# Performance work log

Measured on AMD Instinct MI355X. Metric: run time of the kernel, lower is better.

The kernel has to match this reference:

```python
import jax, jax.numpy as jnp
import numpy as np
import math

NUM_HEADS = 16
D_MODEL = 1024
B, T = 1, 4096


def setup_inputs() -> dict:
    key = jax.random.key(0)
    kx, kq, kk, kv, ko = jax.random.split(key, 5)
    s = 1.0 / math.sqrt(D_MODEL)
    return {
        "x": jax.random.normal(kx, (B, T, D_MODEL), dtype=jnp.float32),
        "Wq": jax.random.normal(kq, (D_MODEL, D_MODEL), dtype=jnp.float32) * s,
        "Wk": jax.random.normal(kk, (D_MODEL, D_MODEL), dtype=jnp.float32) * s,
        "Wv": jax.random.normal(kv, (D_MODEL, D_MODEL), dtype=jnp.float32) * s,
        "Wo": jax.random.normal(ko, (D_MODEL, D_MODEL), dtype=jnp.float32) * s,
    }


def reference(x, Wq, Wk, Wv, Wo):
    # x: (B, T, D); weights stored torch-Linear style: y = x @ W.T
    Bx, Tx, D = x.shape
    H = NUM_HEADS
    dk = D // H
    q = (x @ Wq.T).reshape(Bx, Tx, H, dk)  # (B,T,H,dk)
    k = (x @ Wk.T).reshape(Bx, Tx, H, dk)
    v = (x @ Wv.T).reshape(Bx, Tx, H, dk)
    # scores: (B,H,T,T), scaled dot-product
    scores = jnp.einsum("bthd,bshd->bhts", q, k) / math.sqrt(dk)
    causal_mask = jnp.triu(jnp.ones((Tx, Tx), dtype=bool), k=1)  # True above diag
    scores = jnp.where(causal_mask, jnp.float32(-jnp.inf), scores).astype(jnp.float32)
    attn = jax.nn.softmax(scores, axis=-1)  # fp32 softmax, as in the torch module
    out = jnp.einsum("bhts,bshd->bthd", attn, v).reshape(Bx, Tx, D)
    return out @ Wo.T
```

## Files before the change

kernel.cpp:

```cpp
#include <hip/hip_runtime.h>
#include <hip/hip_bf16.h>
#include <math.h>

typedef __attribute__((ext_vector_type(8)))  __bf16 bf16x8;
typedef __attribute__((ext_vector_type(4)))  __bf16 bf16x4;
typedef __attribute__((ext_vector_type(4)))  float  f32x4;
typedef __attribute__((ext_vector_type(16))) float  f32x16;

static constexpr int T_SEQ = 4096;
static constexpr int DM    = 1024;
static constexpr int NH    = 16;
static constexpr int C2_QB    = 22;
static constexpr int C3_QB    = 44;
static constexpr int SPL_ROWS = T_SEQ - C2_QB * 64;
static constexpr int C3_ROWS  = T_SEQ - C3_QB * 64;
static constexpr int NY = 126;
static constexpr float QSCALE = 0.125f * 1.44269504088896340736f;

__device__ __forceinline__ void gload16(const void* g, void* l) {
    __builtin_amdgcn_global_load_lds(
        (const __attribute__((address_space(1))) unsigned int*)g,
        (__attribute__((address_space(3))) unsigned int*)l,
        16, 0, 0);
}

__device__ __forceinline__ unsigned cvtpk_bf16(float a, float b) {
    unsigned r;
    asm("v_cvt_pk_bf16_f32 %0, %1, %2" : "=v"(r) : "v"(a), "v"(b));
    return r;
}
__device__ __forceinline__ void permswap(unsigned& x, unsigned& y) {
    asm("v_permlane32_swap_b32 %0, %1" : "+v"(x), "+v"(y));
}
__device__ __forceinline__ float xhalf_max(float v) {
    union { float f; unsigned u; } a, b;
    a.f = v; b.f = v;
    asm volatile("" : "+v"(b.u));
    permswap(a.u, b.u);
    return fmaxf(a.f, b.f);
}
__device__ __forceinline__ float xhalf_sum(float v) {
    union { float f; unsigned u; } a, b;
    a.f = v; b.f = v;
    asm volatile("" : "+v"(b.u));
    permswap(a.u, b.u);
    return a.f + b.f;
}

__global__ __launch_bounds__(256)
void cvt_bf16(const float* __restrict__ in, __bf16* __restrict__ out, int n4) {
    int i = blockIdx.x * blockDim.x + threadIdx.x;
    if (i >= n4) return;
    float4 v = ((const float4*)in)[i];
    bf16x4 o;
    o[0] = (__bf16)v.x; o[1] = (__bf16)v.y; o[2] = (__bf16)v.z; o[3] = (__bf16)v.w;
    ((bf16x4*)out)[i] = o;
}

__global__ __launch_bounds__(256)
void cvt4_bf16(const float* __restrict__ a0, const float* __restrict__ a1,
               const float* __restrict__ a2, const float* __restrict__ a3,
               __bf16* __restrict__ o0, __bf16* __restrict__ o1,
               __bf16* __restrict__ o2, __bf16* __restrict__ o3, int n4) {
    int i = blockIdx.x * blockDim.x + threadIdx.x;
    if (i >= n4) return;
    const float* in = blockIdx.y == 0 ? a0 : blockIdx.y == 1 ? a1 : blockIdx.y == 2 ? a2 : a3;
    __bf16* out     = blockIdx.y == 0 ? o0 : blockIdx.y == 1 ? o1 : blockIdx.y == 2 ? o2 : o3;
    float4 v = ((const float4*)in)[i];
    bf16x4 o;
    o[0] = (__bf16)v.x; o[1] = (__bf16)v.y; o[2] = (__bf16)v.z; o[3] = (__bf16)v.w;
    ((bf16x4*)out)[i] = o;
}

template<bool OUT_BF16>
__device__ __forceinline__ void gemm_body(const __bf16* __restrict__ A,
                                          const __bf16* __restrict__ B,
                                          void* __restrict__ Cout,
                                          int N, int K, float scale,
                                          int bx, int by) {
    __shared__ __align__(16) __bf16 Al[128 * 64];
    __shared__ __align__(16) __bf16 Bl[128 * 64];
    const int tid  = threadIdx.x;
    const int lane = tid & 63;
    const int wid  = tid >> 6;
    const int wr   = wid >> 1, wc = wid & 1;
    const int m0   = by * 128, n0 = bx * 128;
    const int r    = lane & 15, g = lane >> 4;

    f32x4 acc[4][4];
    const f32x4 z4 = {0.f, 0.f, 0.f, 0.f};
    #pragma unroll
    for (int i = 0; i < 4; ++i)
        #pragma unroll
        for (int j = 0; j < 4; ++j) acc[i][j] = z4;

    for (int kt = 0; kt < K; kt += 64) {
        __syncthreads();
        #pragma unroll
        for (int p = 0; p < 4; ++p) {
            int u    = p * 256 + tid;
            int row  = u >> 3;
            int col8 = (u & 7) ^ (row & 7);
            gload16(A + (size_t)(m0 + row) * K + kt + col8 * 8,
                    (char*)Al + (p * 256 + wid * 64) * 16);
            gload16(B + (size_t)(n0 + row) * K + kt + col8 * 8,
                    (char*)Bl + (p * 256 + wid * 64) * 16);
        }
        __syncthreads();
        __builtin_amdgcn_s_setprio(1);
        #pragma unroll
        for (int kk = 0; kk < 2; ++kk) {
            bf16x8 af[4], bfr[4];
            #pragma unroll
            for (int mi = 0; mi < 4; ++mi)
                af[mi] = *(const bf16x8*)&Al[(wr * 64 + mi * 16 + r) * 64 + (((kk * 4 + g) ^ (r & 7)) * 8)];
            #pragma unroll
            for (int nj = 0; nj < 4; ++nj)
                bfr[nj] = *(const bf16x8*)&Bl[(wc * 64 + nj * 16 + r) * 64 + (((kk * 4 + g) ^ (r & 7)) * 8)];
            #pragma unroll
            for (int mi = 0; mi < 4; ++mi)
                #pragma unroll
                for (int nj = 0; nj < 4; ++nj)
                    acc[mi][nj] = __builtin_amdgcn_mfma_f32_16x16x32_bf16(af[mi], bfr[nj], acc[mi][nj], 0, 0, 0);
        }
        __builtin_amdgcn_s_setprio(0);
    }
    #pragma unroll
    for (int mi = 0; mi < 4; ++mi)
        #pragma unroll
        for (int nj = 0; nj < 4; ++nj)
            #pragma unroll
            for (int j = 0; j < 4; ++j) {
                int row = m0 + wr * 64 + mi * 16 + g * 4 + j;
                int col = n0 + wc * 64 + nj * 16 + r;
                float v = acc[mi][nj][j] * scale;
                if (OUT_BF16) ((__bf16*)Cout)[(size_t)row * N + col] = (__bf16)v;
                else          ((float*)Cout)[(size_t)row * N + col]  = v;
            }
}

__global__ __launch_bounds__(256)
void gemm_qkv(const __bf16* __restrict__ A,
              const __bf16* __restrict__ W0, const __bf16* __restrict__ W1,
              const __bf16* __restrict__ W2,
              __bf16* __restrict__ O0, __bf16* __restrict__ O1, __bf16* __restrict__ O2) {
    const int z = blockIdx.z;
    const __bf16* B = z == 0 ? W0 : (z == 1 ? W1 : W2);
    __bf16*       C = z == 0 ? O0 : (z == 1 ? O1 : O2);
    float scale = z == 0 ? QSCALE : 1.0f;
    gemm_body<true>(A, B, C, DM, DM, scale, blockIdx.x, blockIdx.y);
}

__global__ __launch_bounds__(256)
void gemm_out(const __bf16* __restrict__ A, const __bf16* __restrict__ B,
              float* __restrict__ C) {
    gemm_body<false>(A, B, C, DM, DM, 1.0f, blockIdx.x, blockIdx.y);
}

__global__ __launch_bounds__(256)
void vtrans(const __bf16* __restrict__ V, __bf16* __restrict__ Vt) {
    __shared__ __bf16 tl[64][72];
    const int tid = threadIdx.x;
    const int t0  = blockIdx.x * 64;
    const int h   = blockIdx.y;
    #pragma unroll
    for (int p = 0; p < 2; ++p) {
        int c = p * 256 + tid, row = c >> 3, col8 = c & 7;
        *(bf16x8*)&tl[row][col8 * 8] =
            *(const bf16x8*)(V + (size_t)(t0 + row) * DM + h * 64 + col8 * 8);
    }
    __syncthreads();
    #pragma unroll
    for (int p = 0; p < 2; ++p) {
        int c = p * 256 + tid, d = c >> 3, tc8 = c & 7;
        bf16x8 o;
        #pragma unroll
        for (int e = 0; e < 8; ++e) o[e] = tl[tc8 * 8 + e][d];
        *(bf16x8*)(Vt + (size_t)(h * 64 + d) * T_SEQ + t0 + tc8 * 8) = o;
    }
}

__global__ __launch_bounds__(128)
void attn_fwd(const __bf16* __restrict__ Q, const __bf16* __restrict__ Kp,
              const __bf16* __restrict__ Vt, __bf16* __restrict__ O,
              __bf16* __restrict__ U0, __bf16* __restrict__ U1,
              __bf16* __restrict__ U2, float* __restrict__ Ml)
{
    __shared__ __align__(16) __bf16 Kl[2][64 * 64];
    __shared__ __align__(16) __bf16 Vl[2][64 * 64];
    const int tid  = threadIdx.x;
    const int lane = tid & 63, wid = tid >> 6;
    const int l31  = lane & 31;
    const int hi   = lane >> 5;
    const int h    = blockIdx.x;
    const int y    = blockIdx.y;
    int qb, chunk, nc;
    if (y < 60)       { qb = 63 - y / 3;        chunk = y % 3;        nc = 3; }
    else if (y < 104) { int s = y - 60; qb = 43 - s / 2; chunk = s % 2; nc = 2; }
    else              { qb = 21 - (y - 104);    chunk = 0;            nc = 1; }
    const int n    = qb + 1;
    const int base = n / nc, rem = n % nc;
    const int t0i  = chunk * base + (chunk < rem ? chunk : rem);
    const int t1i  = t0i + base + (chunk < rem ? 1 : 0) - 1;
    const int qw = qb * 64 + wid * 32;
    const int qg = qw + l31;

    bf16x8 qf[4];
    #pragma unroll
    for (int kd0 = 0; kd0 < 4; ++kd0)
        qf[kd0] = *(const bf16x8*)(Q + (size_t)qg * DM + h * 64 + kd0 * 16 + hi * 8);

    float m_i = -1e30f, l_i = 0.f;
    f32x16 oacc[2];
    #pragma unroll
    for (int d = 0; d < 2; ++d)
        #pragma unroll
        for (int e = 0; e < 16; ++e) oacc[d][e] = 0.f;

    auto stage_lds = [&](int t, int buf) {
        #pragma unroll
        for (int p = 0; p < 4; ++p) {
            int u    = p * 128 + tid;
            int row  = u >> 3;
            int col8 = (u & 7) ^ (row & 7);
            gload16(Kp + (size_t)(t * 64 + row) * DM + h * 64 + col8 * 8,
                    (char*)&Kl[buf][0] + (p * 128 + wid * 64) * 16);
            gload16(Vt + (size_t)(h * 64 + row) * T_SEQ + t * 64 + col8 * 8,
                    (char*)&Vl[buf][0] + (p * 128 + wid * 64) * 16);
        }
    };
    stage_lds(t0i, 0);
    if (t1i > t0i) stage_lds(t0i + 1, 1);
    __syncthreads();

    auto qk = [&](f32x16* sdst, int buf) {
        #pragma unroll
        for (int ksub = 0; ksub < 2; ++ksub) {
            const int row = ksub * 32 + l31;
            f32x16 a;
            #pragma unroll
            for (int e = 0; e < 16; ++e) a[e] = 0.f;
            #pragma unroll
            for (int kd0 = 0; kd0 < 4; ++kd0) {
                bf16x8 kf = *(const bf16x8*)
                    &Kl[buf][(row << 6) + ((((kd0 << 1) + hi) ^ (row & 7)) << 3)];
                a = __builtin_amdgcn_mfma_f32_32x32x16_bf16(kf, qf[kd0], a, 0, 0, 0);
            }
            sdst[ksub] = a;
        }
    };
    auto mask_sf = [&](f32x16* s, int t) {
        const int kb = (t << 6) + 4 * hi;
        #pragma unroll
        for (int ksub = 0; ksub < 2; ++ksub)
            #pragma unroll
            for (int e = 0; e < 16; ++e) {
                int k = kb + ksub * 32 + ((e & 3) + 8 * (e >> 2));
                if (k > qg) s[ksub][e] = -1e30f;
            }
    };

    f32x16 sf[2], sfn[2];
    qk(sf, 0);
    if (t0i == qb) mask_sf(sf, t0i);

    bf16x8 kreg[4], vreg[4];
    for (int t = t0i; t <= t1i; ++t) {
        const int cur = (t - t0i) & 1;
        const bool have_next  = (t + 1 <= t1i);
        const bool have_next2 = (t + 2 <= t1i);
        if (have_next2) {
            const int t2 = t + 2;
            #pragma unroll
            for (int p = 0; p < 4; ++p) {
                int u   = p * 128 + tid;
                int row = u >> 3;
                int c   = u & 7;
                kreg[p] = *(const bf16x8*)(Kp + (size_t)(t2 * 64 + row) * DM + h * 64 + c * 8);
                vreg[p] = *(const bf16x8*)(Vt + (size_t)(h * 64 + row) * T_SEQ + t2 * 64 + c * 8);
            }
        }
        __builtin_amdgcn_s_setprio(1);
        if (have_next) {
            qk(sfn, cur ^ 1);
            if (t + 1 == qb) mask_sf(sfn, t + 1);
        }
        __builtin_amdgcn_s_setprio(0);
        float pm;
        {
            float t0[8];
            #pragma unroll
            for (int e = 0; e < 8; ++e)
                t0[e] = fmaxf(fmaxf(sf[0][e], sf[0][e + 8]), fmaxf(sf[1][e], sf[1][e + 8]));
            #pragma unroll
            for (int s = 4; s > 0; s >>= 1)
                #pragma unroll
                for (int e = 0; e < s; ++e) t0[e] = fmaxf(t0[e], t0[e + s]);
            pm = xhalf_max(t0[0]);
        }
        if (pm > m_i + 8.f) {
            float al = exp2f(m_i - pm);
            m_i = pm;
            l_i *= al;
            #pragma unroll
            for (int d = 0; d < 2; ++d)
                #pragma unroll
                for (int e = 0; e < 16; ++e) oacc[d][e] *= al;
        }
        float p[32];
        #pragma unroll
        for (int i = 0; i < 32; ++i)
            p[i] = exp2f(sf[i >> 4][i & 15] - m_i);
        {
            float s0[8];
            #pragma unroll
            for (int e = 0; e < 8; ++e)
                s0[e] = (p[e] + p[e + 8]) + (p[e + 16] + p[e + 24]);
            #pragma unroll
            for (int s = 4; s > 0; s >>= 1)
                #pragma unroll
                for (int e = 0; e < s; ++e) s0[e] += s0[e + s];
            l_i += xhalf_sum(s0[0]);
        }
        __builtin_amdgcn_s_setprio(1);
        #pragma unroll
        for (int ks = 0; ks < 4; ++ks) {
            unsigned w0 = cvtpk_bf16(p[8 * ks + 0], p[8 * ks + 1]);
            unsigned w1 = cvtpk_bf16(p[8 * ks + 2], p[8 * ks + 3]);
            unsigned w2 = cvtpk_bf16(p[8 * ks + 4], p[8 * ks + 5]);
            unsigned w3 = cvtpk_bf16(p[8 * ks + 6], p[8 * ks + 7]);
            permswap(w0, w2);
            permswap(w1, w3);
            union { unsigned u[4]; bf16x8 v; } pu;
            pu.u[0] = w0; pu.u[1] = w1; pu.u[2] = w2; pu.u[3] = w3;
            #pragma unroll
            for (int dsub = 0; dsub < 2; ++dsub) {
                const int row = dsub * 32 + l31;
                bf16x8 vt = *(const bf16x8*)
                    &Vl[cur][(row << 6) + ((((ks << 1) + hi) ^ (row & 7)) << 3)];
                oacc[dsub] = __builtin_amdgcn_mfma_f32_32x32x16_bf16(vt, pu.v, oacc[dsub], 0, 0, 0);
            }
        }
        __builtin_amdgcn_s_setprio(0);
        if (have_next2) {
            __syncthreads();
            #pragma unroll
            for (int p = 0; p < 4; ++p) {
                int u   = p * 128 + tid;
                int row = u >> 3;
                int c   = u & 7;
                *(bf16x8*)&Kl[cur][(row << 6) + ((c ^ (row & 7)) << 3)] = kreg[p];
                *(bf16x8*)&Vl[cur][(row << 6) + ((c ^ (row & 7)) << 3)] = vreg[p];
            }
            __syncthreads();
        }
        if (have_next) {
            sf[0] = sfn[0];
            sf[1] = sfn[1];
        }
    }
    __syncthreads();
    __bf16* ow = &Kl[0][0] + wid * 2048;
    const float invl = (nc > 1) ? 1.0f : (1.f / l_i);
    #pragma unroll
    for (int dsub = 0; dsub < 2; ++dsub)
        #pragma unroll
        for (int e = 0; e < 16; ++e) {
            int d = dsub * 32 + ((e & 3) + 8 * (e >> 2)) + 4 * hi;
            float v = oacc[dsub][e] * invl;
            int bo = l31 * 128 + ((2 * d) ^ ((l31 & 7) << 4));
            *(__bf16*)((char*)ow + bo) = (__bf16)v;
        }
    if (nc == 1) {
        #pragma unroll
        for (int i = 0; i < 4; ++i) {
            int u  = hi * 4 + i;
            int bo = l31 * 128 + ((u * 16) ^ ((l31 & 7) << 4));
            bf16x8 v8 = *(const bf16x8*)((char*)ow + bo);
            *(bf16x8*)(O + (size_t)qg * DM + h * 64 + u * 8) = v8;
        }
    } else {
        __bf16* Uc = (chunk == 0) ? U0 : (chunk == 1) ? U1 : U2;
        const int rows  = (chunk == 2) ? C3_ROWS : SPL_ROWS;
        const int ridx  = qg - ((chunk == 2) ? C3_QB * 64 : C2_QB * 64);
        #pragma unroll
        for (int i = 0; i < 4; ++i) {
            int u  = hi * 4 + i;
            int bo = l31 * 128 + ((u * 16) ^ ((l31 & 7) << 4));
            bf16x8 v8 = *(const bf16x8*)((char*)ow + bo);
            *(bf16x8*)(Uc + ((size_t)h * rows + ridx) * 64 + u * 8) = v8;
        }
        if (hi == 0) {
            size_t off = (chunk == 0) ? ((size_t)h * SPL_ROWS + (qg - C2_QB * 64))
                       : (chunk == 1) ? ((size_t)NH * SPL_ROWS + (size_t)h * SPL_ROWS + (qg - C2_QB * 64))
                                      : ((size_t)2 * NH * SPL_ROWS + (size_t)h * C3_ROWS + (qg - C3_QB * 64));
            float* mlp = Ml + off * 2;
            mlp[0] = m_i;
            mlp[1] = l_i;
        }
    }
}

__global__ __launch_bounds__(256)
void attn_combine(const __bf16* __restrict__ U0, const __bf16* __restrict__ U1,
                  const __bf16* __restrict__ U2, const float* __restrict__ Ml,
                  __bf16* __restrict__ O) {
    int gid = blockIdx.x * 256 + threadIdx.x;
    int rh  = gid >> 3;
    int e8  = gid & 7;
    int ridx = rh >> 4, h = rh & 15;
    int qg   = C2_QB * 64 + ridx;
    bool has3 = (qg >= C3_QB * 64);
    const float* ml0 = Ml + ((size_t)h * SPL_ROWS + ridx) * 2;
    const float* ml1 = Ml + ((size_t)NH * SPL_ROWS + (size_t)h * SPL_ROWS + ridx) * 2;
    float m0 = ml0[0], l0 = ml0[1], m1 = ml1[0], l1 = ml1[1];
    float m2 = -1e30f, l2 = 0.f;
    if (has3) {
        const float* ml2 = Ml + ((size_t)2 * NH * SPL_ROWS
                                 + (size_t)h * C3_ROWS + (qg - C3_QB * 64)) * 2;
        m2 = ml2[0]; l2 = ml2[1];
    }
    float M  = fmaxf(fmaxf(m0, m1), m2);
    float s0 = exp2f(m0 - M), s1 = exp2f(m1 - M);
    float s2 = has3 ? exp2f(m2 - M) : 0.f;
    float inv = 1.f / (l0 * s0 + l1 * s1 + l2 * s2);
    bf16x8 u0 = *(const bf16x8*)(U0 + ((size_t)h * SPL_ROWS + ridx) * 64 + e8 * 8);
    bf16x8 u1 = *(const bf16x8*)(U1 + ((size_t)h * SPL_ROWS + ridx) * 64 + e8 * 8);
    bf16x8 o;
    if (has3) {
        bf16x8 u2 = *(const bf16x8*)(U2 + ((size_t)h * C3_ROWS + (qg - C3_QB * 64)) * 64 + e8 * 8);
        #pragma unroll
        for (int j = 0; j < 8; ++j)
            o[j] = (__bf16)((((float)u0[j] * s0 + (float)u1[j] * s1) + (float)u2[j] * s2) * inv);
    } else {
        #pragma unroll
        for (int j = 0; j < 8; ++j)
            o[j] = (__bf16)(((float)u0[j] * s0 + (float)u1[j] * s1) * inv);
    }
    *(bf16x8*)(O + (size_t)qg * DM + h * 64 + e8 * 8) = o;
}

extern "C" void kernel_launch(void* const* d_in, const int* in_sizes, int n_in,
                              void* d_out, int out_size, void* d_ws, size_t ws_size,
                              hipStream_t stream) {
    const float* x  = (const float*)d_in[0];
    const float* Wq = (const float*)d_in[1];
    const float* Wk = (const float*)d_in[2];
    const float* Wv = (const float*)d_in[3];
    const float* Wo = (const float*)d_in[4];
    float* out = (float*)d_out;

    char* ws = (char*)d_ws;
    const size_t MB = (size_t)1 << 20;
    __bf16* xb    = (__bf16*)(ws + 0 * MB);
    __bf16* U0B   = (__bf16*)(ws + 0 * MB);
    __bf16* wqb   = (__bf16*)(ws + 8 * MB);
    float*  MlB   = (float*)(ws + 8 * MB);
    __bf16* wkb   = (__bf16*)(ws + 10 * MB);
    __bf16* U2B   = (__bf16*)(ws + 10 * MB);
    __bf16* wvb   = (__bf16*)(ws + 12 * MB);
    __bf16* wob   = (__bf16*)(ws + 14 * MB);
    __bf16* Qb    = (__bf16*)(ws + 16 * MB);
    __bf16* Kb    = (__bf16*)(ws + 24 * MB);
    __bf16* Vb    = (__bf16*)(ws + 32 * MB);
    __bf16* U1B   = (__bf16*)(ws + 32 * MB);
    __bf16* attnb = (__bf16*)(ws + 40 * MB);
    __bf16* VtG   = (__bf16*)(ws + 0 * MB);
    __bf16* VtR   = (__bf16*)(ws + 48 * MB);

    const int nX = T_SEQ * DM / 4;
    const int nW = DM * DM / 4;
    cvt_bf16<<<(nX + 255) / 256, 256, 0, stream>>>(x, xb, nX);
    cvt4_bf16<<<dim3((nW + 255) / 256, 4), 256, 0, stream>>>(Wq, Wk, Wv, Wo,
                                                             wqb, wkb, wvb, wob, nW);

    gemm_qkv<<<dim3(DM / 128, T_SEQ / 128, 3), 256, 0, stream>>>(xb, wqb, wkb, wvb, Qb, Kb, Vb);

    vtrans<<<dim3(T_SEQ / 64, NH), 256, 0, stream>>>(Vb, VtR);

    attn_fwd<<<dim3(NH, NY), 128, 0, stream>>>(Qb, Kb, VtR, attnb, U0B, U1B, U2B, MlB);

    attn_combine<<<(SPL_ROWS * NH * 8) / 256, 256, 0, stream>>>(U0B, U1B, U2B, MlB, attnb);

    gemm_out<<<dim3(DM / 128, T_SEQ / 128), 256, 0, stream>>>(attnb, wob, out);
}
```

Before: 163.5 us.

## Use 128-row query blocks with four waves sharing each K/V tile

The attention kernel now gives each workgroup a 128-query block, served by four waves of 256 threads, in place of a 64-query block with two waves. Each staged K/V tile in LDS is therefore reused by twice as many queries, which halves K/V global and LDS staging traffic per query and halves the grid. Waves whose queries lie entirely above a diagonal tile skip the QK and PV work for it through a per-wave guard. The split-chunk assignment is remapped for the coarser blocks. The risks are fewer workgroups and less occupancy, plus load imbalance, because near the diagonal some waves sit idle while others in the same block do work.

```diff
diff --git a/kernel.cpp b/kernel.cpp
--- a/kernel.cpp
+++ b/kernel.cpp
@@ -14,7 +14,7 @@
 static constexpr int C3_QB    = 44;
 static constexpr int SPL_ROWS = T_SEQ - C2_QB * 64;
 static constexpr int C3_ROWS  = T_SEQ - C3_QB * 64;
-static constexpr int NY = 126;
+static constexpr int NY = 63;
 static constexpr float QSCALE = 0.125f * 1.44269504088896340736f;
 
 __device__ __forceinline__ void gload16(const void* g, void* l) {
@@ -180,7 +180,7 @@
     }
 }
 
-__global__ __launch_bounds__(128)
+__global__ __launch_bounds__(256)
 void attn_fwd(const __bf16* __restrict__ Q, const __bf16* __restrict__ Kp,
               const __bf16* __restrict__ Vt, __bf16* __restrict__ O,
               __bf16* __restrict__ U0, __bf16* __restrict__ U1,
@@ -194,16 +194,16 @@
     const int hi   = lane >> 5;
     const int h    = blockIdx.x;
     const int y    = blockIdx.y;
-    int qb, chunk, nc;
-    if (y < 60)       { qb = 63 - y / 3;        chunk = y % 3;        nc = 3; }
-    else if (y < 104) { int s = y - 60; qb = 43 - s / 2; chunk = s % 2; nc = 2; }
-    else              { qb = 21 - (y - 104);    chunk = 0;            nc = 1; }
-    const int n    = qb + 1;
+    int qblk, chunk, nc;
+    if (y < 30)      { qblk = 31 - y / 3;       chunk = y % 3;        nc = 3; }
+    else if (y < 52) { int s = y - 30; qblk = 21 - s / 2; chunk = s % 2; nc = 2; }
+    else             { qblk = 10 - (y - 52);    chunk = 0;            nc = 1; }
+    const int n    = 2 * qblk + 2;
     const int base = n / nc, rem = n % nc;
     const int t0i  = chunk * base + (chunk < rem ? chunk : rem);
     const int t1i  = t0i + base + (chunk < rem ? 1 : 0) - 1;
-    const int qw = qb * 64 + wid * 32;
-    const int qg = qw + l31;
+    const int qw   = qblk * 128 + wid * 32;
+    const int qg   = qw + l31;
 
     bf16x8 qf[4];
     #pragma unroll
@@ -219,14 +219,14 @@
 
     auto stage_lds = [&](int t, int buf) {
         #pragma unroll
-        for (int p = 0; p < 4; ++p) {
-            int u    = p * 128 + tid;
+        for (int p = 0; p < 2; ++p) {
+            int u    = p * 256 + tid;
             int row  = u >> 3;
             int col8 = (u & 7) ^ (row & 7);
             gload16(Kp + (size_t)(t * 64 + row) * DM + h * 64 + col8 * 8,
-                    (char*)&Kl[buf][0] + (p * 128 + wid * 64) * 16);
+                    (char*)&Kl[buf][0] + (p * 256 + wid * 64) * 16);
             gload16(Vt + (size_t)(h * 64 + row) * T_SEQ + t * 64 + col8 * 8,
-                    (char*)&Vl[buf][0] + (p * 128 + wid * 64) * 16);
+                    (char*)&Vl[buf][0] + (p * 256 + wid * 64) * 16);
         }
     };
     stage_lds(t0i, 0);
@@ -259,12 +259,15 @@
                 if (k > qg) s[ksub][e] = -1e30f;
             }
     };
+    auto haswork = [&](int t) { return (t << 6) <= qw + 31; };
 
     f32x16 sf[2], sfn[2];
-    qk(sf, 0);
-    if (t0i == qb) mask_sf(sf, t0i);
-
-    bf16x8 kreg[4], vreg[4];
+    if (haswork(t0i)) {
+        qk(sf, 0);
+        if ((t0i << 6) + 63 > qw) mask_sf(sf, t0i);
+    }
+
+    bf16x8 kreg[2], vreg[2];
     for (int t = t0i; t <= t1i; ++t) {
         const int cur = (t - t0i) & 1;
         const bool have_next  = (t + 1 <= t1i);
@@ -272,8 +275,8 @@
         if (have_next2) {
             const int t2 = t + 2;
             #pragma unroll
-            for (int p = 0; p < 4; ++p) {
-                int u   = p * 128 + tid;
+            for (int p = 0; p < 2; ++p) {
+                int u   = p * 256 + tid;
                 int row = u >> 3;
                 int c   = u & 7;
                 kreg[p] = *(const bf16x8*)(Kp + (size_t)(t2 * 64 + row) * DM + h * 64 + c * 8);
@@ -281,72 +284,74 @@
             }
         }
         __builtin_amdgcn_s_setprio(1);
-        if (have_next) {
+        if (have_next && haswork(t + 1)) {
             qk(sfn, cur ^ 1);
-            if (t + 1 == qb) mask_sf(sfn, t + 1);
+            if (((t + 1) << 6) + 63 > qw) mask_sf(sfn, t + 1);
         }
         __builtin_amdgcn_s_setprio(0);
-        float pm;
-        {
-            float t0[8];
-            #pragma unroll
-            for (int e = 0; e < 8; ++e)
-                t0[e] = fmaxf(fmaxf(sf[0][e], sf[0][e + 8]), fmaxf(sf[1][e], sf[1][e + 8]));
-            #pragma unroll
-            for (int s = 4; s > 0; s >>= 1)
-                #pragma unroll
-                for (int e = 0; e < s; ++e) t0[e] = fmaxf(t0[e], t0[e + s]);
-            pm = xhalf_max(t0[0]);
-        }
-        if (pm > m_i + 8.f) {
-            float al = exp2f(m_i - pm);
-            m_i = pm;
-            l_i *= al;
-            #pragma unroll
-            for (int d = 0; d < 2; ++d)
-                #pragma unroll
-                for (int e = 0; e < 16; ++e) oacc[d][e] *= al;
-        }
-        float p[32];
-        #pragma unroll
-        for (int i = 0; i < 32; ++i)
-            p[i] = exp2f(sf[i >> 4][i & 15] - m_i);
-        {
-            float s0[8];
-            #pragma unroll
-            for (int e = 0; e < 8; ++e)
-                s0[e] = (p[e] + p[e + 8]) + (p[e + 16] + p[e + 24]);
-            #pragma unroll
-            for (int s = 4; s > 0; s >>= 1)
-                #pragma unroll
-                for (int e = 0; e < s; ++e) s0[e] += s0[e + s];
-            l_i += xhalf_sum(s0[0]);
-        }
-        __builtin_amdgcn_s_setprio(1);
-        #pragma unroll
-        for (int ks = 0; ks < 4; ++ks) {
-            unsigned w0 = cvtpk_bf16(p[8 * ks + 0], p[8 * ks + 1]);
-            unsigned w1 = cvtpk_bf16(p[8 * ks + 2], p[8 * ks + 3]);
-            unsigned w2 = cvtpk_bf16(p[8 * ks + 4], p[8 * ks + 5]);
-            unsigned w3 = cvtpk_bf16(p[8 * ks + 6], p[8 * ks + 7]);
-            permswap(w0, w2);
-            permswap(w1, w3);
-            union { unsigned u[4]; bf16x8 v; } pu;
-            pu.u[0] = w0; pu.u[1] = w1; pu.u[2] = w2; pu.u[3] = w3;
-            #pragma unroll
-            for (int dsub = 0; dsub < 2; ++dsub) {
-                const int row = dsub * 32 + l31;
-                bf16x8 vt = *(const bf16x8*)
-                    &Vl[cur][(row << 6) + ((((ks << 1) + hi) ^ (row & 7)) << 3)];
-                oacc[dsub] = __builtin_amdgcn_mfma_f32_32x32x16_bf16(vt, pu.v, oacc[dsub], 0, 0, 0);
-            }
-        }
-        __builtin_amdgcn_s_setprio(0);
+        if (haswork(t)) {
+            float pm;
+            {
+                float t0[8];
+                #pragma unroll
+                for (int e = 0; e < 8; ++e)
+                    t0[e] = fmaxf(fmaxf(sf[0][e], sf[0][e + 8]), fmaxf(sf[1][e], sf[1][e + 8]));
+                #pragma unroll
+                for (int s = 4; s > 0; s >>= 1)
+                    #pragma unroll
+                    for (int e = 0; e < s; ++e) t0[e] = fmaxf(t0[e], t0[e + s]);
+                pm = xhalf_max(t0[0]);
+            }
+            if (pm > m_i + 8.f) {
+                float al = exp2f(m_i - pm);
+                m_i = pm;
+                l_i *= al;
+                #pragma unroll
+                for (int d = 0; d < 2; ++d)
+                    #pragma unroll
+                    for (int e = 0; e < 16; ++e) oacc[d][e] *= al;
+            }
+            float p[32];
+            #pragma unroll
+            for (int i = 0; i < 32; ++i)
+                p[i] = exp2f(sf[i >> 4][i & 15] - m_i);
+            {
+                float s0[8];
+                #pragma unroll
+                for (int e = 0; e < 8; ++e)
+                    s0[e] = (p[e] + p[e + 8]) + (p[e + 16] + p[e + 24]);
+                #pragma unroll
+                for (int s = 4; s > 0; s >>= 1)
+                    #pragma unroll
+                    for (int e = 0; e < s; ++e) s0[e] += s0[e + s];
+                l_i += xhalf_sum(s0[0]);
+            }
+            __builtin_amdgcn_s_setprio(1);
+            #pragma unroll
+            for (int ks = 0; ks < 4; ++ks) {
+                unsigned w0 = cvtpk_bf16(p[8 * ks + 0], p[8 * ks + 1]);
+                unsigned w1 = cvtpk_bf16(p[8 * ks + 2], p[8 * ks + 3]);
+                unsigned w2 = cvtpk_bf16(p[8 * ks + 4], p[8 * ks + 5]);
+                unsigned w3 = cvtpk_bf16(p[8 * ks + 6], p[8 * ks + 7]);
+                permswap(w0, w2);
+                permswap(w1, w3);
+                union { unsigned u[4]; bf16x8 v; } pu;
+                pu.u[0] = w0; pu.u[1] = w1; pu.u[2] = w2; pu.u[3] = w3;
+                #pragma unroll
+                for (int dsub = 0; dsub < 2; ++dsub) {
+                    const int row = dsub * 32 + l31;
+                    bf16x8 vt = *(const bf16x8*)
+                        &Vl[cur][(row << 6) + ((((ks << 1) + hi) ^ (row & 7)) << 3)];
+                    oacc[dsub] = __builtin_amdgcn_mfma_f32_32x32x16_bf16(vt, pu.v, oacc[dsub], 0, 0, 0);
+                }
+            }
+            __builtin_amdgcn_s_setprio(0);
+        }
         if (have_next2) {
             __syncthreads();
             #pragma unroll
-            for (int p = 0; p < 4; ++p) {
-                int u   = p * 128 + tid;
+            for (int p = 0; p < 2; ++p) {
+                int u   = p * 256 + tid;
                 int row = u >> 3;
                 int c   = u & 7;
                 *(bf16x8*)&Kl[cur][(row << 6) + ((c ^ (row & 7)) << 3)] = kreg[p];
@@ -391,9 +396,9 @@
             *(bf16x8*)(Uc + ((size_t)h * rows + ridx) * 64 + u * 8) = v8;
         }
         if (hi == 0) {
-            size_t off = (chunk == 0) ? ((size_t)h * SPL_ROWS + (qg - C2_QB * 64))
-                       : (chunk == 1) ? ((size_t)NH * SPL_ROWS + (size_t)h * SPL_ROWS + (qg - C2_QB * 64))
-                                      : ((size_t)2 * NH * SPL_ROWS + (size_t)h * C3_ROWS + (qg - C3_QB * 64));
+            size_t off = (chunk == 0) ? ((size_t)h * SPL_ROWS + ridx)
+                       : (chunk == 1) ? ((size_t)(NH + h) * SPL_ROWS + ridx)
+                                      : ((size_t)2 * NH * SPL_ROWS + (size_t)h * C3_ROWS + ridx);
             float* mlp = Ml + off * 2;
             mlp[0] = m_i;
             mlp[1] = l_i;
@@ -412,7 +417,7 @@
     int qg   = C2_QB * 64 + ridx;
     bool has3 = (qg >= C3_QB * 64);
     const float* ml0 = Ml + ((size_t)h * SPL_ROWS + ridx) * 2;
-    const float* ml1 = Ml + ((size_t)NH * SPL_ROWS + (size_t)h * SPL_ROWS + ridx) * 2;
+    const float* ml1 = Ml + ((size_t)(NH + h) * SPL_ROWS + ridx) * 2;
     float m0 = ml0[0], l0 = ml0[1], m1 = ml1[0], l1 = ml1[1];
     float m2 = -1e30f, l2 = 0.f;
     if (has3) {
@@ -465,7 +470,6 @@
     __bf16* Vb    = (__bf16*)(ws + 32 * MB);
     __bf16* U1B   = (__bf16*)(ws + 32 * MB);
     __bf16* attnb = (__bf16*)(ws + 40 * MB);
-    __bf16* VtG   = (__bf16*)(ws + 0 * MB);
     __bf16* VtR   = (__bf16*)(ws + 48 * MB);
 
     const int nX = T_SEQ * DM / 4;
@@ -478,7 +482,7 @@
 
     vtrans<<<dim3(T_SEQ / 64, NH), 256, 0, stream>>>(Vb, VtR);
 
-    attn_fwd<<<dim3(NH, NY), 128, 0, stream>>>(Qb, Kb, VtR, attnb, U0B, U1B, U2B, MlB);
+    attn_fwd<<<dim3(NH, NY), 256, 0, stream>>>(Qb, Kb, VtR, attnb, U0B, U1B, U2B, MlB);
 
     attn_combine<<<(SPL_ROWS * NH * 8) / 256, 256, 0, stream>>>(U0B, U1B, U2B, MlB, attnb);
 
```

Result: slower. 202.8 us (+24.0%).

## Merge conversion kernels and single-buffer K tile in attention LDS

Applied to the files above, without the earlier changes.

Fuses the x and weight fp32-to-bf16 conversions into one launch with a 5-slice grid, removing a kernel launch at the cost of many idle blocks in the weight slices. In the attention kernel, K is now held in a single LDS buffer and the next K tile is loaded into registers and written only after the current QK is consumed, cutting LDS use so more blocks can fit per CU. This adds extra barriers in the prologue and ties K staging more tightly to the compute loop, which may expose load latency. Index expressions for the Ml offsets are simplified.

```diff
diff --git a/kernel.cpp b/kernel.cpp
--- a/kernel.cpp
+++ b/kernel.cpp
@@ -48,24 +48,18 @@
 }
 
 __global__ __launch_bounds__(256)
-void cvt_bf16(const float* __restrict__ in, __bf16* __restrict__ out, int n4) {
+void cvt5_bf16(const float* __restrict__ a0, const float* __restrict__ a1,
+               const float* __restrict__ a2, const float* __restrict__ a3,
+               const float* __restrict__ a4,
+               __bf16* __restrict__ o0, __bf16* __restrict__ o1,
+               __bf16* __restrict__ o2, __bf16* __restrict__ o3,
+               __bf16* __restrict__ o4, int nX4, int nW4) {
+    int y = blockIdx.y;
+    int n4 = (y == 0) ? nX4 : nW4;
     int i = blockIdx.x * blockDim.x + threadIdx.x;
     if (i >= n4) return;
-    float4 v = ((const float4*)in)[i];
-    bf16x4 o;
-    o[0] = (__bf16)v.x; o[1] = (__bf16)v.y; o[2] = (__bf16)v.z; o[3] = (__bf16)v.w;
-    ((bf16x4*)out)[i] = o;
-}
-
-__global__ __launch_bounds__(256)
-void cvt4_bf16(const float* __restrict__ a0, const float* __restrict__ a1,
-               const float* __restrict__ a2, const float* __restrict__ a3,
-               __bf16* __restrict__ o0, __bf16* __restrict__ o1,
-               __bf16* __restrict__ o2, __bf16* __restrict__ o3, int n4) {
-    int i = blockIdx.x * blockDim.x + threadIdx.x;
-    if (i >= n4) return;
-    const float* in = blockIdx.y == 0 ? a0 : blockIdx.y == 1 ? a1 : blockIdx.y == 2 ? a2 : a3;
-    __bf16* out     = blockIdx.y == 0 ? o0 : blockIdx.y == 1 ? o1 : blockIdx.y == 2 ? o2 : o3;
+    const float* in = y == 0 ? a0 : y == 1 ? a1 : y == 2 ? a2 : y == 3 ? a3 : a4;
+    __bf16* out     = y == 0 ? o0 : y == 1 ? o1 : y == 2 ? o2 : y == 3 ? o3 : o4;
     float4 v = ((const float4*)in)[i];
     bf16x4 o;
     o[0] = (__bf16)v.x; o[1] = (__bf16)v.y; o[2] = (__bf16)v.z; o[3] = (__bf16)v.w;
@@ -186,7 +180,7 @@
               __bf16* __restrict__ U0, __bf16* __restrict__ U1,
               __bf16* __restrict__ U2, float* __restrict__ Ml)
 {
-    __shared__ __align__(16) __bf16 Kl[2][64 * 64];
+    __shared__ __align__(16) __bf16 Kl[64 * 64];
     __shared__ __align__(16) __bf16 Vl[2][64 * 64];
     const int tid  = threadIdx.x;
     const int lane = tid & 63, wid = tid >> 6;
@@ -217,23 +211,43 @@
         #pragma unroll
         for (int e = 0; e < 16; ++e) oacc[d][e] = 0.f;
 
-    auto stage_lds = [&](int t, int buf) {
+    bf16x8 kreg[4], vreg[4];
+    auto stageK_lds = [&](int t) {
         #pragma unroll
         for (int p = 0; p < 4; ++p) {
             int u    = p * 128 + tid;
             int row  = u >> 3;
             int col8 = (u & 7) ^ (row & 7);
             gload16(Kp + (size_t)(t * 64 + row) * DM + h * 64 + col8 * 8,
-                    (char*)&Kl[buf][0] + (p * 128 + wid * 64) * 16);
+                    (char*)&Kl[0] + (p * 128 + wid * 64) * 16);
+        }
+    };
+    auto stageV_lds = [&](int t, int buf) {
+        #pragma unroll
+        for (int p = 0; p < 4; ++p) {
+            int u    = p * 128 + tid;
+            int row  = u >> 3;
+            int col8 = (u & 7) ^ (row & 7);
             gload16(Vt + (size_t)(h * 64 + row) * T_SEQ + t * 64 + col8 * 8,
                     (char*)&Vl[buf][0] + (p * 128 + wid * 64) * 16);
         }
     };
-    stage_lds(t0i, 0);
-    if (t1i > t0i) stage_lds(t0i + 1, 1);
-    __syncthreads();
-
-    auto qk = [&](f32x16* sdst, int buf) {
+    auto ldK = [&](int t) {
+        #pragma unroll
+        for (int p = 0; p < 4; ++p) {
+            int u = p * 128 + tid, row = u >> 3, c = u & 7;
+            kreg[p] = *(const bf16x8*)(Kp + (size_t)(t * 64 + row) * DM + h * 64 + c * 8);
+        }
+    };
+    auto wrK = [&]() {
+        #pragma unroll
+        for (int p = 0; p < 4; ++p) {
+            int u = p * 128 + tid, row = u >> 3, c = u & 7;
+            *(bf16x8*)&Kl[(row << 6) + ((c ^ (row & 7)) << 3)] = kreg[p];
+        }
+    };
+
+    auto qk = [&](f32x16* sdst) {
         #pragma unroll
         for (int ksub = 0; ksub < 2; ++ksub) {
             const int row = ksub * 32 + l31;
@@ -243,7 +257,7 @@
             #pragma unroll
             for (int kd0 = 0; kd0 < 4; ++kd0) {
                 bf16x8 kf = *(const bf16x8*)
-                    &Kl[buf][(row << 6) + ((((kd0 << 1) + hi) ^ (row & 7)) << 3)];
+                    &Kl[(row << 6) + ((((kd0 << 1) + hi) ^ (row & 7)) << 3)];
                 a = __builtin_amdgcn_mfma_f32_32x32x16_bf16(kf, qf[kd0], a, 0, 0, 0);
             }
             sdst[ksub] = a;
@@ -260,11 +274,18 @@
             }
     };
 
+    stageK_lds(t0i);
+    stageV_lds(t0i, 0);
+    const bool multi = (t1i > t0i);
+    if (multi) { stageV_lds(t0i + 1, 1); ldK(t0i + 1); }
+    __syncthreads();
     f32x16 sf[2], sfn[2];
-    qk(sf, 0);
+    qk(sf);
     if (t0i == qb) mask_sf(sf, t0i);
-
-    bf16x8 kreg[4], vreg[4];
+    __syncthreads();
+    if (multi) wrK();
+    __syncthreads();
+
     for (int t = t0i; t <= t1i; ++t) {
         const int cur = (t - t0i) & 1;
         const bool have_next  = (t + 1 <= t1i);
@@ -282,7 +303,7 @@
         }
         __builtin_amdgcn_s_setprio(1);
         if (have_next) {
-            qk(sfn, cur ^ 1);
+            qk(sfn);
             if (t + 1 == qb) mask_sf(sfn, t + 1);
         }
         __builtin_amdgcn_s_setprio(0);
@@ -344,12 +365,12 @@
         __builtin_amdgcn_s_setprio(0);
         if (have_next2) {
             __syncthreads();
+            wrK();
             #pragma unroll
             for (int p = 0; p < 4; ++p) {
                 int u   = p * 128 + tid;
                 int row = u >> 3;
                 int c   = u & 7;
-                *(bf16x8*)&Kl[cur][(row << 6) + ((c ^ (row & 7)) << 3)] = kreg[p];
                 *(bf16x8*)&Vl[cur][(row << 6) + ((c ^ (row & 7)) << 3)] = vreg[p];
             }
             __syncthreads();
@@ -360,7 +381,7 @@
         }
     }
     __syncthreads();
-    __bf16* ow = &Kl[0][0] + wid * 2048;
+    __bf16* ow = &Kl[0] + wid * 2048;
     const float invl = (nc > 1) ? 1.0f : (1.f / l_i);
     #pragma unroll
     for (int dsub = 0; dsub < 2; ++dsub)
@@ -391,9 +412,9 @@
             *(bf16x8*)(Uc + ((size_t)h * rows + ridx) * 64 + u * 8) = v8;
         }
         if (hi == 0) {
-            size_t off = (chunk == 0) ? ((size_t)h * SPL_ROWS + (qg - C2_QB * 64))
-                       : (chunk == 1) ? ((size_t)NH * SPL_ROWS + (size_t)h * SPL_ROWS + (qg - C2_QB * 64))
-                                      : ((size_t)2 * NH * SPL_ROWS + (size_t)h * C3_ROWS + (qg - C3_QB * 64));
+            size_t off = (chunk == 0) ? ((size_t)h * SPL_ROWS + ridx)
+                       : (chunk == 1) ? ((size_t)(NH + h) * SPL_ROWS + ridx)
+                                      : ((size_t)2 * NH * SPL_ROWS + (size_t)h * C3_ROWS + ridx);
             float* mlp = Ml + off * 2;
             mlp[0] = m_i;
             mlp[1] = l_i;
@@ -412,7 +433,7 @@
     int qg   = C2_QB * 64 + ridx;
     bool has3 = (qg >= C3_QB * 64);
     const float* ml0 = Ml + ((size_t)h * SPL_ROWS + ridx) * 2;
-    const float* ml1 = Ml + ((size_t)NH * SPL_ROWS + (size_t)h * SPL_ROWS + ridx) * 2;
+    const float* ml1 = Ml + ((size_t)(NH + h) * SPL_ROWS + ridx) * 2;
     float m0 = ml0[0], l0 = ml0[1], m1 = ml1[0], l1 = ml1[1];
     float m2 = -1e30f, l2 = 0.f;
     if (has3) {
@@ -465,14 +486,12 @@
     __bf16* Vb    = (__bf16*)(ws + 32 * MB);
     __bf16* U1B   = (__bf16*)(ws + 32 * MB);
     __bf16* attnb = (__bf16*)(ws + 40 * MB);
-    __bf16* VtG   = (__bf16*)(ws + 0 * MB);
     __bf16* VtR   = (__bf16*)(ws + 48 * MB);
 
-    const int nX = T_SEQ * DM / 4;
-    const int nW = DM * DM / 4;
-    cvt_bf16<<<(nX + 255) / 256, 256, 0, stream>>>(x, xb, nX);
-    cvt4_bf16<<<dim3((nW + 255) / 256, 4), 256, 0, stream>>>(Wq, Wk, Wv, Wo,
-                                                             wqb, wkb, wvb, wob, nW);
+    const int nX4 = T_SEQ * DM / 4;
+    const int nW4 = DM * DM / 4;
+    cvt5_bf16<<<dim3((nX4 + 255) / 256, 5), 256, 0, stream>>>(
+        x, Wq, Wk, Wv, Wo, xb, wqb, wkb, wvb, wob, nX4, nW4);
 
     gemm_qkv<<<dim3(DM / 128, T_SEQ / 128, 3), 256, 0, stream>>>(xb, wqb, wkb, wvb, Qb, Kb, Vb);
 
```

After: 190.3 us. 1.16x slower.
